# Kernel optimization log

Hardware: AMD Instinct MI355X
Metric: run time of the kernel (lower is better)

## Reference

```python
import jax, jax.numpy as jnp
import numpy as np

NUM_CLASSES = 22
SKIP = 20            # skip_pixels: stride over flattened pixel index
N_STEPS = 200        # discretized steps along each voting ray
STEP = 4.0           # pixels per ray step
INLIER_T = 0.9       # inlier_threshold on direction dot-product
LABEL_T = 500.0      # label_threshold: min #pixels of a class to be valid


def _hough_forward(label_2d, vertex_pred, extents, poses, meta_data):
    B, H, W = label_2d.shape
    C = NUM_CLASSES
    HW = H * W

    # ---- strided pixel sampling (skip_pixels) ----
    idx = jnp.arange(0, HW, SKIP)                      # [P]
    P = idx.shape[0]
    ys = (idx // W).astype(jnp.float32)                # [P]
    xs = (idx % W).astype(jnp.float32)
    labels = label_2d.reshape(B, HW)[:, idx].astype(jnp.int32)   # [B,P]
    vp = vertex_pred.reshape(B, HW, C, 3)[:, idx]                # [B,P,C,3]
    # pick each pixel's predicted (dx,dy,z) for its own class label
    sel = jnp.take_along_axis(
        vp, jnp.broadcast_to(labels[:, :, None, None], (B, P, 1, 3)), axis=2
    )[:, :, 0]                                                   # [B,P,3]
    d = sel[..., :2]
    dn = d / (jnp.linalg.norm(d, axis=-1, keepdims=True) + 1e-9)  # unit dir [B,P,2]
    z = sel[..., 2]                                               # [B,P]
    fg = labels > 0                                               # foreground mask

    # ---- ray voting into per-class Hough accumulator ----
    t = (jnp.arange(N_STEPS, dtype=jnp.float32) + 1.0) * STEP     # [T]
    cx = xs[None, :, None] + dn[..., 0:1] * t[None, None, :]      # [B,P,T]
    cy = ys[None, :, None] + dn[..., 1:2] * t[None, None, :]
    cxi = jnp.round(cx).astype(jnp.int32)
    cyi = jnp.round(cy).astype(jnp.int32)
    inb = (cxi >= 0) & (cxi < W) & (cyi >= 0) & (cyi < H) & fg[..., None]
    cxi = jnp.clip(cxi, 0, W - 1)
    cyi = jnp.clip(cyi, 0, H - 1)
    bidx = jnp.arange(B, dtype=jnp.int32)[:, None, None]
    flat = ((bidx * C + labels[:, :, None]) * H + cyi) * W + cxi  # [B,P,T]
    hough = jnp.zeros((B * C * HW,), jnp.float32)
    hough = hough.at[flat.reshape(-1)].add(inb.reshape(-1).astype(jnp.float32))
    hough = hough.reshape(B, C, H, W)

    # ---- per-class peak ----
    hflat = hough.reshape(B, C, HW)
    vmax = hflat.max(-1)                               # [B,C]
    pk = jnp.argmax(hflat, axis=-1).astype(jnp.int32)  # [B,C]
    pky = (pk // W).astype(jnp.float32)
    pkx = (pk % W).astype(jnp.float32)

    # ---- validity: enough labeled pixels for the class ----
    b2 = jnp.arange(B, dtype=jnp.int32)[:, None]
    counts = jnp.zeros((B, C), jnp.float32).at[
        jnp.broadcast_to(b2, (B, HW)).reshape(-1),
        label_2d.reshape(-1).astype(jnp.int32),
    ].add(1.0)                                          # [B,C] full-res pixel counts
    cls_ids = jnp.arange(C, dtype=jnp.float32)
    valid = (counts >= LABEL_T) & (cls_ids[None, :] > 0)  # [B,C]

    # ---- inlier selection + inlier-averaged depth ----
    cx_c = jnp.take_along_axis(pkx, labels, axis=1)    # [B,P] peak of pixel's class
    cy_c = jnp.take_along_axis(pky, labels, axis=1)
    dvec = jnp.stack([cx_c - xs[None, :], cy_c - ys[None, :]], axis=-1)
    dvec = dvec / (jnp.linalg.norm(dvec, axis=-1, keepdims=True) + 1e-9)
    dot = jnp.sum(dn * dvec, axis=-1)                  # [B,P]
    inl = (fg & (dot > INLIER_T)).astype(jnp.float32)  # [B,P]
    bP = jnp.broadcast_to(b2, (B, P)).reshape(-1)
    z_sum = jnp.zeros((B, C), jnp.float32).at[bP, labels.reshape(-1)].add((z * inl).reshape(-1))
    n_inl = jnp.zeros((B, C), jnp.float32).at[bP, labels.reshape(-1)].add(inl.reshape(-1))
    depth = z_sum / jnp.maximum(n_inl, 1.0)            # [B,C]
    z_safe = jnp.where(jnp.abs(depth) > 1e-3, depth, 1.0)

    # ---- bbox from extents + intrinsics ----
    fx = meta_data[:, 0:1]                             # [B,1]
    fy = meta_data[:, 4:5]
    diam = jnp.linalg.norm(extents, axis=-1)[None, :]  # [1,C]
    half_w = 0.5 * diam * fx / z_safe
    half_h = 0.5 * diam * fy / z_safe
    vmask = valid.astype(jnp.float32)
    rois = jnp.stack([
        jnp.broadcast_to(b2.astype(jnp.float32), (B, C)),
        jnp.broadcast_to(cls_ids[None, :], (B, C)),
        pkx - half_w, pky - half_h, pkx + half_w, pky + half_h,
        vmax,
    ], axis=-1) * vmask[..., None]                     # [B,C,7]

    # ---- pose init: identity quaternion + backprojected translation ----
    Kinv = meta_data[:, 9:18].reshape(B, 3, 3)
    hom = jnp.stack([pkx, pky, jnp.ones_like(pkx)], axis=-1)      # [B,C,3]
    ray = jnp.einsum('bij,bcj->bci', Kinv, hom)
    T = depth[..., None] * ray                                    # [B,C,3]
    quat = jnp.broadcast_to(jnp.array([1.0, 0.0, 0.0, 0.0], jnp.float32), (B, C, 4))
    pose_out = jnp.concatenate([quat, T], axis=-1) * vmask[..., None]  # [B,C,7]

    return jnp.concatenate([rois, pose_out], axis=-1)  # [B,C,14]


def setup_inputs() -> dict:
    key = jax.random.key(0)
    k1, k2, k3 = jax.random.split(key, 3)
    B, H, W = 2, 480, 640
    label_2d = jax.random.randint(k1, (B, H, W), 0, NUM_CLASSES, dtype=jnp.int32)
    vertex_pred = jax.random.normal(k2, (B, H, W, 3 * NUM_CLASSES), dtype=jnp.float32)
    extents = jax.random.uniform(k3, (NUM_CLASSES, 3), minval=0.05, maxval=0.3, dtype=jnp.float32)
    poses = jnp.zeros((B, 13), jnp.float32)
    K = np.array([[1066.778, 0, 312.9869], [0, 1067.487, 241.3109], [0, 0, 1]], dtype=np.float32)
    Kinv = np.linalg.pinv(K).astype(np.float32)
    md = np.zeros((B, 48), np.float32)
    md[:, 0:9] = K.flatten()
    md[:, 9:18] = Kinv.flatten()
    meta_data = jnp.asarray(md)
    return {"label_2d": label_2d, "vertex_pred": vertex_pred, "extents": extents,
            "poses": poses, "meta_data": meta_data}


def reference(label_2d, vertex_pred, extents, poses, meta_data):
    return _hough_forward(label_2d, vertex_pred, extents, poses, meta_data)
```

## Files before the change

### kernel.cpp

```cpp
#include <hip/hip_runtime.h>
#include <math.h>

#define C_      22
#define SKIP_   20
#define NSTEP_  200
#define STEP_   4.0f
#define INL_T_  0.9f
#define LAB_T_  500
#define B_      2
#define H_      480
#define W_      640
#define HW_     (H_ * W_)
#define P_      (HW_ / SKIP_)

#define TS_       64
#define TILES_X_  (W_ / TS_)
#define NTILES_Y_ 8
#define NTILES_   (TILES_X_ * NTILES_Y_)
#define NPLANES_  (B_ * (C_ - 1))
#define NPT_      (NPLANES_ * NTILES_)
#define CAP_      2048

#define SUB_A_    8
#define SEG_LEN_  (NSTEP_ / SUB_A_)
#define PA_BLOCKS_    ((B_ * P_ * SUB_A_) / 256)
#define HIST_BLOCKS_  ((B_ * HW_) / (256 * 4))
#define INL_BLOCKS_   ((B_ * P_) / 256)

#define KEY_INIT_ 0x00000000FFFFFFFFull

__device__ __forceinline__ void emit_run(unsigned int* cnt, uint4* lists, int pt,
                                         int xi, int yi, int i0, int i1,
                                         float dnx, float dny) {
    unsigned slot = atomicAdd(&cnt[pt], 1u);
    if (slot < CAP_) {
        uint4 r;
        r.x = (unsigned)xi | ((unsigned)yi << 16);
        r.y = (unsigned)i0 | ((unsigned)i1 << 8);
        r.z = __float_as_uint(dnx);
        r.w = __float_as_uint(dny);
        lists[(size_t)pt * CAP_ + slot] = r;
    }
}

__global__ __launch_bounds__(256) void binray_count_kernel(const int* __restrict__ label,
                                                           const float* __restrict__ vp,
                                                           unsigned int* __restrict__ cnt,
                                                           uint4* __restrict__ lists,
                                                           int* __restrict__ counts,
                                                           unsigned long long* __restrict__ key) {
    if (blockIdx.x < PA_BLOCKS_) {
        int tid = blockIdx.x * 256 + threadIdx.x;
        int pt  = tid >> 3;
        int sub = tid & 7;
        int b   = pt / P_;
        int pi  = pt - b * P_;
        int idx = pi * SKIP_;
        int lab = label[b * HW_ + idx];
        if (lab <= 0) return;
        int xi = idx % W_, yi = idx / W_;
        float xs = (float)xi, ys = (float)yi;
        const float* s = vp + ((size_t)(b * HW_ + idx) * (C_ * 3)) + lab * 3;
        float dx = s[0], dy = s[1];
        float nrm = sqrtf(__fadd_rn(__fmul_rn(dx, dx), __fmul_rn(dy, dy))) + 1e-9f;
        float dnx = dx / nrm, dny = dy / nrm;
        int base = (b * (C_ - 1) + (lab - 1)) * NTILES_;
        int curTile = -1, runStart = 0;
        bool entered = false;
        int iBeg = sub * SEG_LEN_, iEnd = iBeg + SEG_LEN_;
        for (int i = iBeg; i < iEnd; ++i) {
            float t = (float)(i + 1) * STEP_;
            float cx = __fadd_rn(xs, __fmul_rn(dnx, t));
            float cy = __fadd_rn(ys, __fmul_rn(dny, t));
            float cxr = rintf(cx);
            float cyr = rintf(cy);
            int tl2 = -1;
            if (cxr >= 0.0f && cxr <= (float)(W_ - 1) && cyr >= 0.0f && cyr <= (float)(H_ - 1))
                tl2 = (((int)cyr) >> 6) * TILES_X_ + (((int)cxr) >> 6);
            if (tl2 != curTile) {
                if (curTile >= 0)
                    emit_run(cnt, lists, base + curTile, xi, yi, runStart, i - 1, dnx, dny);
                curTile = tl2;
                runStart = i;
            }
            if (tl2 >= 0) entered = true;
            else if (entered) break;
        }
        if (curTile >= 0)
            emit_run(cnt, lists, base + curTile, xi, yi, runStart, iEnd - 1, dnx, dny);
    } else {
        __shared__ int h[C_];
        int cb  = blockIdx.x - PA_BLOCKS_;
        if (cb == 0 && threadIdx.x < B_ * C_)
            key[threadIdx.x] = KEY_INIT_;
        const int bpb = HW_ / 1024;
        int b   = cb / bpb;
        int off = (cb % bpb) * 1024 + threadIdx.x * 4;
        if (threadIdx.x < C_) h[threadIdx.x] = 0;
        __syncthreads();
        int4 l4 = *(const int4*)(label + b * HW_ + off);
        atomicAdd(&h[l4.x], 1);
        atomicAdd(&h[l4.y], 1);
        atomicAdd(&h[l4.z], 1);
        atomicAdd(&h[l4.w], 1);
        __syncthreads();
        if (threadIdx.x < C_) {
            int v = h[threadIdx.x];
            if (v) atomicAdd(&counts[b * C_ + threadIdx.x], v);
        }
    }
}

__global__ __launch_bounds__(256) void raster_argmax_kernel(const unsigned int* __restrict__ cnt,
                                                            const uint4* __restrict__ lists,
                                                            unsigned long long* __restrict__ key) {
    __shared__ unsigned int tile[TS_ * TS_ / 2];
    __shared__ unsigned int sv[256];
    __shared__ int          si[256];
    int pt = blockIdx.x;
    int n = (int)cnt[pt];
    if (n == 0) return;
    if (n > CAP_) n = CAP_;
    {
        uint4* t4 = (uint4*)tile;
        t4[threadIdx.x]       = make_uint4(0u, 0u, 0u, 0u);
        t4[threadIdx.x + 256] = make_uint4(0u, 0u, 0u, 0u);
    }
    __syncthreads();
    int p  = pt / NTILES_;
    int tl = pt % NTILES_;
    int b = p / (C_ - 1);
    int c = p % (C_ - 1) + 1;
    int x0 = (tl % TILES_X_) * TS_;
    int y0 = (tl / TILES_X_) * TS_;
    const uint4* lst = lists + (size_t)pt * CAP_;
    int hwv = threadIdx.x >> 5, ln = threadIdx.x & 31;
    for (int r = hwv; r < n; r += 8) {
        uint4 rec = lst[r];
        int i0 = (int)(rec.y & 0xFFu), i1 = (int)((rec.y >> 8) & 0xFFu);
        float xs = (float)(rec.x & 0xFFFFu);
        float ys = (float)(rec.x >> 16);
        float dnx = __uint_as_float(rec.z);
        float dny = __uint_as_float(rec.w);
        for (int i = i0 + ln; i <= i1; i += 32) {
            float t = (float)(i + 1) * STEP_;
            float cx = __fadd_rn(xs, __fmul_rn(dnx, t));
            float cy = __fadd_rn(ys, __fmul_rn(dny, t));
            int lx = (int)rintf(cx) - x0;
            int ly = (int)rintf(cy) - y0;
            int cell = ly * TS_ + lx;
            atomicAdd(&tile[cell >> 1], 1u << ((cell & 1) * 16));
        }
    }
    __syncthreads();
    unsigned bv = 0u; int bi = 0;
    {
        unsigned w0 = tile[threadIdx.x];
        bv = w0 & 0xFFFFu; bi = threadIdx.x * 2;
        unsigned hi = w0 >> 16;
        if (hi > bv) { bv = hi; bi = threadIdx.x * 2 + 1; }
    }
    #pragma unroll
    for (int j = 1; j < 8; ++j) {
        int ix = threadIdx.x + j * 256;
        unsigned w = tile[ix];
        unsigned lo = w & 0xFFFFu, hi = w >> 16;
        if (lo > bv) { bv = lo; bi = ix * 2; }
        if (hi > bv) { bv = hi; bi = ix * 2 + 1; }
    }
    sv[threadIdx.x] = bv; si[threadIdx.x] = bi;
    __syncthreads();
    for (int s = 128; s > 0; s >>= 1) {
        if (threadIdx.x < s) {
            unsigned ov = sv[threadIdx.x + s]; int oi = si[threadIdx.x + s];
            if (ov > sv[threadIdx.x] || (ov == sv[threadIdx.x] && oi < si[threadIdx.x])) {
                sv[threadIdx.x] = ov; si[threadIdx.x] = oi;
            }
        }
        __syncthreads();
    }
    if (threadIdx.x == 0) {
        int ly = si[0] >> 6, lx = si[0] & 63;
        unsigned gidx = (unsigned)((y0 + ly) * W_ + (x0 + lx));
        unsigned long long k = ((unsigned long long)sv[0] << 32)
                             | (unsigned long long)(0xFFFFFFFFu - gidx);
        atomicMax(&key[b * C_ + c], k);
    }
}

__global__ __launch_bounds__(256) void inlier_finalize_kernel(const int* __restrict__ label,
                                                              const float* __restrict__ vp,
                                                              const unsigned long long* __restrict__ key,
                                                              float* __restrict__ z_sum,
                                                              float* __restrict__ n_inl,
                                                              int* __restrict__ counts,
                                                              const float* __restrict__ extents,
                                                              const float* __restrict__ meta,
                                                              unsigned int* __restrict__ done,
                                                              float* __restrict__ out) {
    __shared__ float zs[C_];
    __shared__ float ns[C_];
    __shared__ int last_flag;
    const int bpb = P_ / 256;
    int b  = blockIdx.x / bpb;
    int pi = (blockIdx.x % bpb) * 256 + threadIdx.x;
    if (threadIdx.x < C_) { zs[threadIdx.x] = 0.0f; ns[threadIdx.x] = 0.0f; }
    __syncthreads();
    int idx = pi * SKIP_;
    int lab = label[b * HW_ + idx];
    if (lab > 0) {
        float ys = (float)(idx / W_);
        float xs = (float)(idx % W_);
        const float* s = vp + ((size_t)(b * HW_ + idx) * (C_ * 3)) + lab * 3;
        float dx = s[0], dy = s[1], z = s[2];
        float nrm = sqrtf(__fadd_rn(__fmul_rn(dx, dx), __fmul_rn(dy, dy))) + 1e-9f;
        float dnx = dx / nrm, dny = dy / nrm;
        unsigned long long k = key[b * C_ + lab];
        int pkv = (int)(0xFFFFFFFFu - (unsigned int)(k & 0xFFFFFFFFull));
        float pkx = (float)(pkv % W_), pky = (float)(pkv / W_);
        float dvx = __fsub_rn(pkx, xs), dvy = __fsub_rn(pky, ys);
        float nrm2 = sqrtf(__fadd_rn(__fmul_rn(dvx, dvx), __fmul_rn(dvy, dvy))) + 1e-9f;
        dvx /= nrm2; dvy /= nrm2;
        float dot = __fadd_rn(__fmul_rn(dnx, dvx), __fmul_rn(dny, dvy));
        if (dot > INL_T_) {
            atomicAdd(&zs[lab], z);
            atomicAdd(&ns[lab], 1.0f);
        }
    }
    __syncthreads();
    if (threadIdx.x < C_) {
        if (ns[threadIdx.x] != 0.0f) {
            atomicAdd(&z_sum[b * C_ + threadIdx.x], zs[threadIdx.x]);
            atomicAdd(&n_inl[b * C_ + threadIdx.x], ns[threadIdx.x]);
        }
    }
    if (threadIdx.x == 0) {
        __threadfence();
        unsigned prev = atomicAdd(done, 1u);
        last_flag = (prev == (unsigned)(INL_BLOCKS_ - 1)) ? 1 : 0;
    }
    __syncthreads();
    if (!last_flag) return;
    __threadfence();
    int t = threadIdx.x;
    if (t >= B_ * C_) return;
    int bb = t / C_, c = t % C_;
    float* o = out + t * 14;
    int   cnt_t  = atomicAdd(&counts[t], 0);
    float zsum_t = atomicAdd(&z_sum[t], 0.0f);
    float ninl_t = atomicAdd(&n_inl[t], 0.0f);
    unsigned long long k = atomicAdd((unsigned long long*)&key[0] + t, 0ull);
    bool valid = (cnt_t >= LAB_T_) && (c > 0);
    if (!valid) {
        #pragma unroll
        for (int k2 = 0; k2 < 14; ++k2) o[k2] = 0.0f;
        return;
    }
    float depth = zsum_t / fmaxf(ninl_t, 1.0f);
    float z_safe = (fabsf(depth) > 0.001f) ? depth : 1.0f;
    float fx = meta[bb * 48 + 0];
    float fy = meta[bb * 48 + 4];
    const float* e = extents + c * 3;
    float diam = sqrtf(e[0]*e[0] + e[1]*e[1] + e[2]*e[2]);
    float vmax = (float)(unsigned int)(k >> 32);
    int pkv = (int)(0xFFFFFFFFu - (unsigned int)(k & 0xFFFFFFFFull));
    float pkx = (float)(pkv % W_), pky = (float)(pkv / W_);
    float half_w = ((0.5f * diam) * fx) / z_safe;
    float half_h = ((0.5f * diam) * fy) / z_safe;
    o[0] = (float)bb;
    o[1] = (float)c;
    o[2] = pkx - half_w;
    o[3] = pky - half_h;
    o[4] = pkx + half_w;
    o[5] = pky + half_h;
    o[6] = vmax;
    const float* Ki = meta + bb * 48 + 9;
    float rx = Ki[0]*pkx + Ki[1]*pky + Ki[2];
    float ry = Ki[3]*pkx + Ki[4]*pky + Ki[5];
    float rz = Ki[6]*pkx + Ki[7]*pky + Ki[8];
    o[7]  = 1.0f;
    o[8]  = 0.0f;
    o[9]  = 0.0f;
    o[10] = 0.0f;
    o[11] = depth * rx;
    o[12] = depth * ry;
    o[13] = depth * rz;
}

extern "C" void kernel_launch(void* const* d_in, const int* in_sizes, int n_in,
                              void* d_out, int out_size, void* d_ws, size_t ws_size,
                              hipStream_t stream) {
    const int*   label   = (const int*)d_in[0];
    const float* vp      = (const float*)d_in[1];
    const float* extents = (const float*)d_in[2];
    const float* meta    = (const float*)d_in[4];
    float* out = (float*)d_out;

    char* ws = (char*)d_ws;
    size_t off = 0;
    unsigned int* cnt = (unsigned int*)(ws + off);  off += NPT_ * sizeof(unsigned int);
    int*   counts = (int*)(ws + off);   off += B_ * C_ * sizeof(int);
    float* z_sum  = (float*)(ws + off); off += B_ * C_ * sizeof(float);
    float* n_inl  = (float*)(ws + off); off += B_ * C_ * sizeof(float);
    unsigned int* done = (unsigned int*)(ws + off); off += sizeof(unsigned int);
    size_t zero_bytes = off;
    off = (off + 15) & ~(size_t)15;
    unsigned long long* key = (unsigned long long*)(ws + off);
    off += B_ * C_ * sizeof(unsigned long long);
    off = (off + 15) & ~(size_t)15;
    uint4* lists = (uint4*)(ws + off);

    hipMemsetAsync(d_ws, 0, zero_bytes, stream);

    binray_count_kernel<<<PA_BLOCKS_ + HIST_BLOCKS_, 256, 0, stream>>>(label, vp, cnt, lists, counts, key);
    raster_argmax_kernel<<<NPT_, 256, 0, stream>>>(cnt, lists, key);
    inlier_finalize_kernel<<<INL_BLOCKS_, 256, 0, stream>>>(label, vp, key, z_sum, n_inl,
                                                            counts, extents, meta, done, out);
}
```

Before: 259.4 us.

## Replace memset and three launches with two kernels using in-kernel flag synchronization

Drops the workspace memset by having block 0 of the first kernel zero the counters and publish magic flags. The other blocks spin on those flags before doing their work. The first kernel becomes persistent with a fixed 1024-block grid, and the raster/argmax and inlier/finalize kernels merge into one launch whose inlier blocks spin until every raster tile has signalled completion. The aim is to save launch and memset overhead, but it relies on forward progress of spinning blocks and adds busy-wait costs.

```diff
diff --git a/kernel.cpp b/kernel.cpp
--- a/kernel.cpp
+++ b/kernel.cpp
@@ -25,9 +25,13 @@
 #define SEG_LEN_  (NSTEP_ / SUB_A_)
 #define PA_BLOCKS_    ((B_ * P_ * SUB_A_) / 256)
 #define HIST_BLOCKS_  ((B_ * HW_) / (256 * 4))
+#define UNITS1_       (PA_BLOCKS_ + HIST_BLOCKS_)
+#define GRID1_        1024
 #define INL_BLOCKS_   ((B_ * P_) / 256)
 
 #define KEY_INIT_ 0x00000000FFFFFFFFull
+#define MAGIC1_   0x9E3779B9u
+#define MAGIC2_   0x61C8C646u
 
 __device__ __forceinline__ void emit_run(unsigned int* cnt, uint4* lists, int pt,
                                          int xi, int yi, int i0, int i1,
@@ -43,168 +47,217 @@
     }
 }
 
-__global__ __launch_bounds__(256) void binray_count_kernel(const int* __restrict__ label,
-                                                           const float* __restrict__ vp,
-                                                           unsigned int* __restrict__ cnt,
-                                                           uint4* __restrict__ lists,
-                                                           int* __restrict__ counts,
-                                                           unsigned long long* __restrict__ key) {
-    if (blockIdx.x < PA_BLOCKS_) {
-        int tid = blockIdx.x * 256 + threadIdx.x;
-        int pt  = tid >> 3;
-        int sub = tid & 7;
-        int b   = pt / P_;
-        int pi  = pt - b * P_;
-        int idx = pi * SKIP_;
-        int lab = label[b * HW_ + idx];
-        if (lab <= 0) return;
-        int xi = idx % W_, yi = idx / W_;
-        float xs = (float)xi, ys = (float)yi;
-        const float* s = vp + ((size_t)(b * HW_ + idx) * (C_ * 3)) + lab * 3;
-        float dx = s[0], dy = s[1];
-        float nrm = sqrtf(__fadd_rn(__fmul_rn(dx, dx), __fmul_rn(dy, dy))) + 1e-9f;
-        float dnx = dx / nrm, dny = dy / nrm;
-        int base = (b * (C_ - 1) + (lab - 1)) * NTILES_;
-        int curTile = -1, runStart = 0;
-        bool entered = false;
-        int iBeg = sub * SEG_LEN_, iEnd = iBeg + SEG_LEN_;
-        for (int i = iBeg; i < iEnd; ++i) {
-            float t = (float)(i + 1) * STEP_;
-            float cx = __fadd_rn(xs, __fmul_rn(dnx, t));
-            float cy = __fadd_rn(ys, __fmul_rn(dny, t));
-            float cxr = rintf(cx);
-            float cyr = rintf(cy);
-            int tl2 = -1;
-            if (cxr >= 0.0f && cxr <= (float)(W_ - 1) && cyr >= 0.0f && cyr <= (float)(H_ - 1))
-                tl2 = (((int)cyr) >> 6) * TILES_X_ + (((int)cxr) >> 6);
-            if (tl2 != curTile) {
+__global__ __launch_bounds__(256, 4) void binray_init_kernel(const int* __restrict__ label,
+                                                             const float* __restrict__ vp,
+                                                             unsigned int* __restrict__ cnt,
+                                                             uint4* __restrict__ lists,
+                                                             int* __restrict__ counts,
+                                                             float* __restrict__ z_sum,
+                                                             float* __restrict__ n_inl,
+                                                             unsigned int* __restrict__ done,
+                                                             unsigned int* __restrict__ rdone,
+                                                             unsigned int* __restrict__ flags,
+                                                             unsigned long long* __restrict__ key) {
+    __shared__ int h[C_];
+    const int tid = threadIdx.x;
+    if (blockIdx.x == 0) {
+        for (int i = tid; i < NPT_; i += 256) cnt[i] = 0u;
+        if (tid < B_ * C_) {
+            counts[tid] = 0;
+            z_sum[tid] = 0.0f;
+            n_inl[tid] = 0.0f;
+            key[tid] = KEY_INIT_;
+        }
+        if (tid == 0) { *done = 0u; *rdone = 0u; }
+        __syncthreads();
+        __threadfence();
+        if (tid == 0) {
+            atomicExch(&flags[0], MAGIC1_);
+            atomicExch(&flags[1], MAGIC2_);
+        }
+        __syncthreads();
+    } else {
+        if (tid == 0) {
+            while (true) {
+                unsigned f1 = atomicAdd(&flags[0], 0u);
+                unsigned f2 = atomicAdd(&flags[1], 0u);
+                if (f1 == MAGIC1_ && f2 == MAGIC2_) break;
+                __builtin_amdgcn_s_sleep(2);
+            }
+            __threadfence();
+        }
+        __syncthreads();
+    }
+
+    for (int u = blockIdx.x; u < UNITS1_; u += GRID1_) {
+        if (u < PA_BLOCKS_) {
+            int t0  = u * 256 + tid;
+            int pt  = t0 >> 3;
+            int sub = t0 & 7;
+            int b   = pt / P_;
+            int pi  = pt - b * P_;
+            int idx = pi * SKIP_;
+            int lab = label[b * HW_ + idx];
+            if (lab > 0) {
+                int xi = idx % W_, yi = idx / W_;
+                float xs = (float)xi, ys = (float)yi;
+                const float* s = vp + ((size_t)(b * HW_ + idx) * (C_ * 3)) + lab * 3;
+                float dx = s[0], dy = s[1];
+                float nrm = sqrtf(__fadd_rn(__fmul_rn(dx, dx), __fmul_rn(dy, dy))) + 1e-9f;
+                float dnx = dx / nrm, dny = dy / nrm;
+                int base = (b * (C_ - 1) + (lab - 1)) * NTILES_;
+                int curTile = -1, runStart = 0;
+                bool entered = false;
+                int iBeg = sub * SEG_LEN_, iEnd = iBeg + SEG_LEN_;
+                for (int i = iBeg; i < iEnd; ++i) {
+                    float t = (float)(i + 1) * STEP_;
+                    float cx = __fadd_rn(xs, __fmul_rn(dnx, t));
+                    float cy = __fadd_rn(ys, __fmul_rn(dny, t));
+                    float cxr = rintf(cx);
+                    float cyr = rintf(cy);
+                    int tl2 = -1;
+                    if (cxr >= 0.0f && cxr <= (float)(W_ - 1) && cyr >= 0.0f && cyr <= (float)(H_ - 1))
+                        tl2 = (((int)cyr) >> 6) * TILES_X_ + (((int)cxr) >> 6);
+                    if (tl2 != curTile) {
+                        if (curTile >= 0)
+                            emit_run(cnt, lists, base + curTile, xi, yi, runStart, i - 1, dnx, dny);
+                        curTile = tl2;
+                        runStart = i;
+                    }
+                    if (tl2 >= 0) entered = true;
+                    else if (entered) break;
+                }
                 if (curTile >= 0)
-                    emit_run(cnt, lists, base + curTile, xi, yi, runStart, i - 1, dnx, dny);
-                curTile = tl2;
-                runStart = i;
-            }
-            if (tl2 >= 0) entered = true;
-            else if (entered) break;
-        }
-        if (curTile >= 0)
-            emit_run(cnt, lists, base + curTile, xi, yi, runStart, iEnd - 1, dnx, dny);
-    } else {
-        __shared__ int h[C_];
-        int cb  = blockIdx.x - PA_BLOCKS_;
-        if (cb == 0 && threadIdx.x < B_ * C_)
-            key[threadIdx.x] = KEY_INIT_;
-        const int bpb = HW_ / 1024;
-        int b   = cb / bpb;
-        int off = (cb % bpb) * 1024 + threadIdx.x * 4;
-        if (threadIdx.x < C_) h[threadIdx.x] = 0;
-        __syncthreads();
-        int4 l4 = *(const int4*)(label + b * HW_ + off);
-        atomicAdd(&h[l4.x], 1);
-        atomicAdd(&h[l4.y], 1);
-        atomicAdd(&h[l4.z], 1);
-        atomicAdd(&h[l4.w], 1);
-        __syncthreads();
-        if (threadIdx.x < C_) {
-            int v = h[threadIdx.x];
-            if (v) atomicAdd(&counts[b * C_ + threadIdx.x], v);
+                    emit_run(cnt, lists, base + curTile, xi, yi, runStart, iEnd - 1, dnx, dny);
+            }
+        } else {
+            int cb  = u - PA_BLOCKS_;
+            const int bpb = HW_ / 1024;
+            int b   = cb / bpb;
+            int off = (cb % bpb) * 1024 + tid * 4;
+            if (tid < C_) h[tid] = 0;
+            __syncthreads();
+            int4 l4 = *(const int4*)(label + b * HW_ + off);
+            atomicAdd(&h[l4.x], 1);
+            atomicAdd(&h[l4.y], 1);
+            atomicAdd(&h[l4.z], 1);
+            atomicAdd(&h[l4.w], 1);
+            __syncthreads();
+            if (tid < C_) {
+                int v = h[tid];
+                if (v) atomicAdd(&counts[b * C_ + tid], v);
+            }
+            __syncthreads();
         }
     }
 }
 
-__global__ __launch_bounds__(256) void raster_argmax_kernel(const unsigned int* __restrict__ cnt,
-                                                            const uint4* __restrict__ lists,
-                                                            unsigned long long* __restrict__ key) {
-    __shared__ unsigned int tile[TS_ * TS_ / 2];
-    __shared__ unsigned int sv[256];
-    __shared__ int          si[256];
-    int pt = blockIdx.x;
-    int n = (int)cnt[pt];
-    if (n == 0) return;
-    if (n > CAP_) n = CAP_;
-    {
-        uint4* t4 = (uint4*)tile;
-        t4[threadIdx.x]       = make_uint4(0u, 0u, 0u, 0u);
-        t4[threadIdx.x + 256] = make_uint4(0u, 0u, 0u, 0u);
+__global__ __launch_bounds__(256) void raster_inlier_finalize_kernel(
+        const unsigned int* __restrict__ cnt, const uint4* __restrict__ lists,
+        unsigned long long* __restrict__ key,
+        const int* __restrict__ label, const float* __restrict__ vp,
+        float* __restrict__ z_sum, float* __restrict__ n_inl,
+        int* __restrict__ counts, const float* __restrict__ extents,
+        const float* __restrict__ meta,
+        unsigned int* __restrict__ done, unsigned int* __restrict__ rdone,
+        unsigned int* __restrict__ flags, float* __restrict__ out) {
+    __shared__ union {
+        struct { unsigned int tile[TS_ * TS_ / 2]; unsigned int sv[256]; int si[256]; } rb;
+        struct { float zs[C_]; float ns[C_]; unsigned long long kk[C_]; int last_flag; } in;
+    } sm;
+    const int tid = threadIdx.x;
+
+    if (blockIdx.x < NPT_) {
+        int pt = blockIdx.x;
+        int n = (int)cnt[pt];
+        if (n == 0) {
+            if (tid == 0) atomicAdd(rdone, 1u);
+            return;
+        }
+        if (n > CAP_) n = CAP_;
+        {
+            uint4* t4 = (uint4*)sm.rb.tile;
+            t4[tid]       = make_uint4(0u, 0u, 0u, 0u);
+            t4[tid + 256] = make_uint4(0u, 0u, 0u, 0u);
+        }
+        __syncthreads();
+        int p  = pt / NTILES_;
+        int tl = pt % NTILES_;
+        int b = p / (C_ - 1);
+        int c = p % (C_ - 1) + 1;
+        int x0 = (tl % TILES_X_) * TS_;
+        int y0 = (tl / TILES_X_) * TS_;
+        const uint4* lst = lists + (size_t)pt * CAP_;
+        int hwv = tid >> 5, ln = tid & 31;
+        for (int r = hwv; r < n; r += 8) {
+            uint4 rec = lst[r];
+            int i0 = (int)(rec.y & 0xFFu), i1 = (int)((rec.y >> 8) & 0xFFu);
+            float xs = (float)(rec.x & 0xFFFFu);
+            float ys = (float)(rec.x >> 16);
+            float dnx = __uint_as_float(rec.z);
+            float dny = __uint_as_float(rec.w);
+            for (int i = i0 + ln; i <= i1; i += 32) {
+                float t = (float)(i + 1) * STEP_;
+                float cx = __fadd_rn(xs, __fmul_rn(dnx, t));
+                float cy = __fadd_rn(ys, __fmul_rn(dny, t));
+                int lx = (int)rintf(cx) - x0;
+                int ly = (int)rintf(cy) - y0;
+                int cell = ly * TS_ + lx;
+                atomicAdd(&sm.rb.tile[cell >> 1], 1u << ((cell & 1) * 16));
+            }
+        }
+        __syncthreads();
+        unsigned bv = 0u; int bi = 0;
+        {
+            unsigned w0 = sm.rb.tile[tid];
+            bv = w0 & 0xFFFFu; bi = tid * 2;
+            unsigned hi = w0 >> 16;
+            if (hi > bv) { bv = hi; bi = tid * 2 + 1; }
+        }
+        #pragma unroll
+        for (int j = 1; j < 8; ++j) {
+            int ix = tid + j * 256;
+            unsigned w = sm.rb.tile[ix];
+            unsigned lo = w & 0xFFFFu, hi = w >> 16;
+            if (lo > bv) { bv = lo; bi = ix * 2; }
+            if (hi > bv) { bv = hi; bi = ix * 2 + 1; }
+        }
+        sm.rb.sv[tid] = bv; sm.rb.si[tid] = bi;
+        __syncthreads();
+        for (int s = 128; s > 0; s >>= 1) {
+            if (tid < s) {
+                unsigned ov = sm.rb.sv[tid + s]; int oi = sm.rb.si[tid + s];
+                if (ov > sm.rb.sv[tid] || (ov == sm.rb.sv[tid] && oi < sm.rb.si[tid])) {
+                    sm.rb.sv[tid] = ov; sm.rb.si[tid] = oi;
+                }
+            }
+            __syncthreads();
+        }
+        if (tid == 0) {
+            int ly = sm.rb.si[0] >> 6, lx = sm.rb.si[0] & 63;
+            unsigned gidx = (unsigned)((y0 + ly) * W_ + (x0 + lx));
+            unsigned long long k = ((unsigned long long)sm.rb.sv[0] << 32)
+                                 | (unsigned long long)(0xFFFFFFFFu - gidx);
+            atomicMax(&key[b * C_ + c], k);
+            __threadfence();
+            atomicAdd(rdone, 1u);
+        }
+        return;
+    }
+
+    int ib = blockIdx.x - NPT_;
+    const int bpb = P_ / 256;
+    int b  = ib / bpb;
+    int pi = (ib % bpb) * 256 + tid;
+    if (tid == 0) {
+        while (atomicAdd(rdone, 0u) < (unsigned)NPT_) __builtin_amdgcn_s_sleep(8);
+        __threadfence();
     }
     __syncthreads();
-    int p  = pt / NTILES_;
-    int tl = pt % NTILES_;
-    int b = p / (C_ - 1);
-    int c = p % (C_ - 1) + 1;
-    int x0 = (tl % TILES_X_) * TS_;
-    int y0 = (tl / TILES_X_) * TS_;
-    const uint4* lst = lists + (size_t)pt * CAP_;
-    int hwv = threadIdx.x >> 5, ln = threadIdx.x & 31;
-    for (int r = hwv; r < n; r += 8) {
-        uint4 rec = lst[r];
-        int i0 = (int)(rec.y & 0xFFu), i1 = (int)((rec.y >> 8) & 0xFFu);
-        float xs = (float)(rec.x & 0xFFFFu);
-        float ys = (float)(rec.x >> 16);
-        float dnx = __uint_as_float(rec.z);
-        float dny = __uint_as_float(rec.w);
-        for (int i = i0 + ln; i <= i1; i += 32) {
-            float t = (float)(i + 1) * STEP_;
-            float cx = __fadd_rn(xs, __fmul_rn(dnx, t));
-            float cy = __fadd_rn(ys, __fmul_rn(dny, t));
-            int lx = (int)rintf(cx) - x0;
-            int ly = (int)rintf(cy) - y0;
-            int cell = ly * TS_ + lx;
-            atomicAdd(&tile[cell >> 1], 1u << ((cell & 1) * 16));
-        }
-    }
-    __syncthreads();
-    unsigned bv = 0u; int bi = 0;
-    {
-        unsigned w0 = tile[threadIdx.x];
-        bv = w0 & 0xFFFFu; bi = threadIdx.x * 2;
-        unsigned hi = w0 >> 16;
-        if (hi > bv) { bv = hi; bi = threadIdx.x * 2 + 1; }
-    }
-    #pragma unroll
-    for (int j = 1; j < 8; ++j) {
-        int ix = threadIdx.x + j * 256;
-        unsigned w = tile[ix];
-        unsigned lo = w & 0xFFFFu, hi = w >> 16;
-        if (lo > bv) { bv = lo; bi = ix * 2; }
-        if (hi > bv) { bv = hi; bi = ix * 2 + 1; }
-    }
-    sv[threadIdx.x] = bv; si[threadIdx.x] = bi;
-    __syncthreads();
-    for (int s = 128; s > 0; s >>= 1) {
-        if (threadIdx.x < s) {
-            unsigned ov = sv[threadIdx.x + s]; int oi = si[threadIdx.x + s];
-            if (ov > sv[threadIdx.x] || (ov == sv[threadIdx.x] && oi < si[threadIdx.x])) {
-                sv[threadIdx.x] = ov; si[threadIdx.x] = oi;
-            }
-        }
-        __syncthreads();
-    }
-    if (threadIdx.x == 0) {
-        int ly = si[0] >> 6, lx = si[0] & 63;
-        unsigned gidx = (unsigned)((y0 + ly) * W_ + (x0 + lx));
-        unsigned long long k = ((unsigned long long)sv[0] << 32)
-                             | (unsigned long long)(0xFFFFFFFFu - gidx);
-        atomicMax(&key[b * C_ + c], k);
-    }
-}
-
-__global__ __launch_bounds__(256) void inlier_finalize_kernel(const int* __restrict__ label,
-                                                              const float* __restrict__ vp,
-                                                              const unsigned long long* __restrict__ key,
-                                                              float* __restrict__ z_sum,
-                                                              float* __restrict__ n_inl,
-                                                              int* __restrict__ counts,
-                                                              const float* __restrict__ extents,
-                                                              const float* __restrict__ meta,
-                                                              unsigned int* __restrict__ done,
-                                                              float* __restrict__ out) {
-    __shared__ float zs[C_];
-    __shared__ float ns[C_];
-    __shared__ int last_flag;
-    const int bpb = P_ / 256;
-    int b  = blockIdx.x / bpb;
-    int pi = (blockIdx.x % bpb) * 256 + threadIdx.x;
-    if (threadIdx.x < C_) { zs[threadIdx.x] = 0.0f; ns[threadIdx.x] = 0.0f; }
+    if (tid < C_) {
+        sm.in.zs[tid] = 0.0f; sm.in.ns[tid] = 0.0f;
+        sm.in.kk[tid] = atomicAdd(&key[b * C_ + tid], 0ull);
+    }
     __syncthreads();
     int idx = pi * SKIP_;
     int lab = label[b * HW_ + idx];
@@ -215,7 +268,7 @@
         float dx = s[0], dy = s[1], z = s[2];
         float nrm = sqrtf(__fadd_rn(__fmul_rn(dx, dx), __fmul_rn(dy, dy))) + 1e-9f;
         float dnx = dx / nrm, dny = dy / nrm;
-        unsigned long long k = key[b * C_ + lab];
+        unsigned long long k = sm.in.kk[lab];
         int pkv = (int)(0xFFFFFFFFu - (unsigned int)(k & 0xFFFFFFFFull));
         float pkx = (float)(pkv % W_), pky = (float)(pkv / W_);
         float dvx = __fsub_rn(pkx, xs), dvy = __fsub_rn(pky, ys);
@@ -223,33 +276,37 @@
         dvx /= nrm2; dvy /= nrm2;
         float dot = __fadd_rn(__fmul_rn(dnx, dvx), __fmul_rn(dny, dvy));
         if (dot > INL_T_) {
-            atomicAdd(&zs[lab], z);
-            atomicAdd(&ns[lab], 1.0f);
+            atomicAdd(&sm.in.zs[lab], z);
+            atomicAdd(&sm.in.ns[lab], 1.0f);
         }
     }
     __syncthreads();
-    if (threadIdx.x < C_) {
-        if (ns[threadIdx.x] != 0.0f) {
-            atomicAdd(&z_sum[b * C_ + threadIdx.x], zs[threadIdx.x]);
-            atomicAdd(&n_inl[b * C_ + threadIdx.x], ns[threadIdx.x]);
-        }
-    }
-    if (threadIdx.x == 0) {
+    if (tid < C_) {
+        if (sm.in.ns[tid] != 0.0f) {
+            atomicAdd(&z_sum[b * C_ + tid], sm.in.zs[tid]);
+            atomicAdd(&n_inl[b * C_ + tid], sm.in.ns[tid]);
+        }
+    }
+    if (tid == 0) {
         __threadfence();
         unsigned prev = atomicAdd(done, 1u);
-        last_flag = (prev == (unsigned)(INL_BLOCKS_ - 1)) ? 1 : 0;
+        sm.in.last_flag = (prev == (unsigned)(INL_BLOCKS_ - 1)) ? 1 : 0;
     }
     __syncthreads();
-    if (!last_flag) return;
+    if (!sm.in.last_flag) return;
     __threadfence();
-    int t = threadIdx.x;
+    if (tid == 0) {
+        atomicExch(&flags[0], 0u);
+        atomicExch(&flags[1], 0u);
+    }
+    int t = tid;
     if (t >= B_ * C_) return;
     int bb = t / C_, c = t % C_;
     float* o = out + t * 14;
     int   cnt_t  = atomicAdd(&counts[t], 0);
     float zsum_t = atomicAdd(&z_sum[t], 0.0f);
     float ninl_t = atomicAdd(&n_inl[t], 0.0f);
-    unsigned long long k = atomicAdd((unsigned long long*)&key[0] + t, 0ull);
+    unsigned long long k = atomicAdd(&key[t], 0ull);
     bool valid = (cnt_t >= LAB_T_) && (c > 0);
     if (!valid) {
         #pragma unroll
@@ -302,18 +359,18 @@
     int*   counts = (int*)(ws + off);   off += B_ * C_ * sizeof(int);
     float* z_sum  = (float*)(ws + off); off += B_ * C_ * sizeof(float);
     float* n_inl  = (float*)(ws + off); off += B_ * C_ * sizeof(float);
-    unsigned int* done = (unsigned int*)(ws + off); off += sizeof(unsigned int);
-    size_t zero_bytes = off;
+    unsigned int* done  = (unsigned int*)(ws + off); off += sizeof(unsigned int);
+    unsigned int* rdone = (unsigned int*)(ws + off); off += sizeof(unsigned int);
+    unsigned int* flags = (unsigned int*)(ws + off); off += 2 * sizeof(unsigned int);
     off = (off + 15) & ~(size_t)15;
     unsigned long long* key = (unsigned long long*)(ws + off);
     off += B_ * C_ * sizeof(unsigned long long);
     off = (off + 15) & ~(size_t)15;
     uint4* lists = (uint4*)(ws + off);
 
-    hipMemsetAsync(d_ws, 0, zero_bytes, stream);
-
-    binray_count_kernel<<<PA_BLOCKS_ + HIST_BLOCKS_, 256, 0, stream>>>(label, vp, cnt, lists, counts, key);
-    raster_argmax_kernel<<<NPT_, 256, 0, stream>>>(cnt, lists, key);
-    inlier_finalize_kernel<<<INL_BLOCKS_, 256, 0, stream>>>(label, vp, key, z_sum, n_inl,
-                                                            counts, extents, meta, done, out);
+    binray_init_kernel<<<GRID1_, 256, 0, stream>>>(label, vp, cnt, lists, counts,
+                                                   z_sum, n_inl, done, rdone, flags, key);
+    raster_inlier_finalize_kernel<<<NPT_ + INL_BLOCKS_, 256, 0, stream>>>(
+        cnt, lists, key, label, vp, z_sum, n_inl, counts, extents, meta,
+        done, rdone, flags, out);
 }
```

Result: slower. 398.3 us (+53.5%).

## Fuse inlier voting into raster kernel via per-class pixel lists and last-block finalize

Applied to the files above, without the earlier changes.

The first kernel now also writes each foreground pixel's position, depth and unit direction into a per-class compacted list. The inlier/finalize kernel is removed. The last raster block to finish for each class plane, detected with a per-plane done counter, reads that list to accumulate inlier depth and write the output row. The argmax reduction uses wave shuffles instead of a shared-memory tree. This removes one kernel launch and avoids re-reading labels and the strided vertex predictions, at the cost of extra global writes in the first kernel, and the per-class inlier pass now runs serially inside a single block.

```diff
diff --git a/kernel.cpp b/kernel.cpp
--- a/kernel.cpp
+++ b/kernel.cpp
@@ -25,7 +25,6 @@
 #define SEG_LEN_  (NSTEP_ / SUB_A_)
 #define PA_BLOCKS_    ((B_ * P_ * SUB_A_) / 256)
 #define HIST_BLOCKS_  ((B_ * HW_) / (256 * 4))
-#define INL_BLOCKS_   ((B_ * P_) / 256)
 
 #define KEY_INIT_ 0x00000000FFFFFFFFull
 
@@ -48,7 +47,10 @@
                                                            unsigned int* __restrict__ cnt,
                                                            uint4* __restrict__ lists,
                                                            int* __restrict__ counts,
-                                                           unsigned long long* __restrict__ key) {
+                                                           unsigned int* __restrict__ cls_cnt,
+                                                           uint4* __restrict__ cls,
+                                                           unsigned long long* __restrict__ key,
+                                                           float* __restrict__ out) {
     if (blockIdx.x < PA_BLOCKS_) {
         int tid = blockIdx.x * 256 + threadIdx.x;
         int pt  = tid >> 3;
@@ -64,7 +66,20 @@
         float dx = s[0], dy = s[1];
         float nrm = sqrtf(__fadd_rn(__fmul_rn(dx, dx), __fmul_rn(dy, dy))) + 1e-9f;
         float dnx = dx / nrm, dny = dy / nrm;
-        int base = (b * (C_ - 1) + (lab - 1)) * NTILES_;
+        int p = b * (C_ - 1) + (lab - 1);
+        int base = p * NTILES_;
+        if (sub == 0) {
+            float z = s[2];
+            unsigned slot = atomicAdd(&cls_cnt[p], 1u);
+            if (slot < (unsigned)P_) {
+                uint4 r;
+                r.x = (unsigned)xi | ((unsigned)yi << 16);
+                r.y = __float_as_uint(z);
+                r.z = __float_as_uint(dnx);
+                r.w = __float_as_uint(dny);
+                cls[(size_t)p * P_ + slot] = r;
+            }
+        }
         int curTile = -1, runStart = 0;
         bool entered = false;
         int iBeg = sub * SEG_LEN_, iEnd = iBeg + SEG_LEN_;
@@ -91,8 +106,14 @@
     } else {
         __shared__ int h[C_];
         int cb  = blockIdx.x - PA_BLOCKS_;
-        if (cb == 0 && threadIdx.x < B_ * C_)
-            key[threadIdx.x] = KEY_INIT_;
+        if (cb == 0) {
+            if (threadIdx.x < B_ * C_)
+                key[threadIdx.x] = KEY_INIT_;
+            else if (threadIdx.x < B_ * C_ + 14)
+                out[threadIdx.x - B_ * C_] = 0.0f;
+            else if (threadIdx.x < B_ * C_ + 28)
+                out[C_ * 14 + (threadIdx.x - B_ * C_ - 14)] = 0.0f;
+        }
         const int bpb = HW_ / 1024;
         int b   = cb / bpb;
         int off = (cb % bpb) * 1024 + threadIdx.x * 4;
@@ -111,146 +132,140 @@
     }
 }
 
-__global__ __launch_bounds__(256) void raster_argmax_kernel(const unsigned int* __restrict__ cnt,
-                                                            const uint4* __restrict__ lists,
-                                                            unsigned long long* __restrict__ key) {
-    __shared__ unsigned int tile[TS_ * TS_ / 2];
-    __shared__ unsigned int sv[256];
-    __shared__ int          si[256];
+__global__ __launch_bounds__(256) void raster_finalize_kernel(
+        const unsigned int* __restrict__ cnt, const uint4* __restrict__ lists,
+        unsigned long long* __restrict__ key,
+        const uint4* __restrict__ cls, const unsigned int* __restrict__ cls_cnt,
+        unsigned int* __restrict__ pdone,
+        const int* __restrict__ counts, const float* __restrict__ extents,
+        const float* __restrict__ meta, float* __restrict__ out) {
+    __shared__ union {
+        struct { unsigned int tile[TS_ * TS_ / 2]; unsigned int sv[4]; int si[4]; } rb;
+        struct { float zp[4]; float np[4]; } in;
+    } sm;
+    __shared__ int last_flag;
+    __shared__ unsigned long long kbro;
+    const int tid = threadIdx.x;
+
     int pt = blockIdx.x;
-    int n = (int)cnt[pt];
-    if (n == 0) return;
-    if (n > CAP_) n = CAP_;
-    {
-        uint4* t4 = (uint4*)tile;
-        t4[threadIdx.x]       = make_uint4(0u, 0u, 0u, 0u);
-        t4[threadIdx.x + 256] = make_uint4(0u, 0u, 0u, 0u);
-    }
-    __syncthreads();
     int p  = pt / NTILES_;
     int tl = pt % NTILES_;
     int b = p / (C_ - 1);
     int c = p % (C_ - 1) + 1;
     int x0 = (tl % TILES_X_) * TS_;
     int y0 = (tl / TILES_X_) * TS_;
-    const uint4* lst = lists + (size_t)pt * CAP_;
-    int hwv = threadIdx.x >> 5, ln = threadIdx.x & 31;
-    for (int r = hwv; r < n; r += 8) {
-        uint4 rec = lst[r];
-        int i0 = (int)(rec.y & 0xFFu), i1 = (int)((rec.y >> 8) & 0xFFu);
+
+    int n = (int)cnt[pt];
+    if (n > CAP_) n = CAP_;
+    if (n > 0) {
+        {
+            uint4* t4 = (uint4*)sm.rb.tile;
+            t4[tid]       = make_uint4(0u, 0u, 0u, 0u);
+            t4[tid + 256] = make_uint4(0u, 0u, 0u, 0u);
+        }
+        __syncthreads();
+        const uint4* lst = lists + (size_t)pt * CAP_;
+        int hwv = tid >> 5, ln = tid & 31;
+        for (int r = hwv; r < n; r += 8) {
+            uint4 rec = lst[r];
+            int i0 = (int)(rec.y & 0xFFu), i1 = (int)((rec.y >> 8) & 0xFFu);
+            float xs = (float)(rec.x & 0xFFFFu);
+            float ys = (float)(rec.x >> 16);
+            float dnx = __uint_as_float(rec.z);
+            float dny = __uint_as_float(rec.w);
+            for (int i = i0 + ln; i <= i1; i += 32) {
+                float t = (float)(i + 1) * STEP_;
+                float cx = __fadd_rn(xs, __fmul_rn(dnx, t));
+                float cy = __fadd_rn(ys, __fmul_rn(dny, t));
+                int lx = (int)rintf(cx) - x0;
+                int ly = (int)rintf(cy) - y0;
+                int cell = ly * TS_ + lx;
+                atomicAdd(&sm.rb.tile[cell >> 1], 1u << ((cell & 1) * 16));
+            }
+        }
+        __syncthreads();
+        unsigned bv = 0u; int bi = 0;
+        {
+            unsigned w0 = sm.rb.tile[tid];
+            bv = w0 & 0xFFFFu; bi = tid * 2;
+            unsigned hi = w0 >> 16;
+            if (hi > bv) { bv = hi; bi = tid * 2 + 1; }
+        }
+        #pragma unroll
+        for (int j = 1; j < 8; ++j) {
+            int ix = tid + j * 256;
+            unsigned w = sm.rb.tile[ix];
+            unsigned lo = w & 0xFFFFu, hi = w >> 16;
+            if (lo > bv) { bv = lo; bi = ix * 2; }
+            if (hi > bv) { bv = hi; bi = ix * 2 + 1; }
+        }
+        #pragma unroll
+        for (int s = 1; s < 64; s <<= 1) {
+            unsigned ov = (unsigned)__shfl_xor((int)bv, s);
+            int      oi = __shfl_xor(bi, s);
+            if (ov > bv || (ov == bv && oi < bi)) { bv = ov; bi = oi; }
+        }
+        if ((tid & 63) == 0) { sm.rb.sv[tid >> 6] = bv; sm.rb.si[tid >> 6] = bi; }
+        __syncthreads();
+        if (tid == 0) {
+            unsigned fbv = sm.rb.sv[0]; int fbi = sm.rb.si[0];
+            #pragma unroll
+            for (int w = 1; w < 4; ++w) {
+                unsigned ov = sm.rb.sv[w]; int oi = sm.rb.si[w];
+                if (ov > fbv || (ov == fbv && oi < fbi)) { fbv = ov; fbi = oi; }
+            }
+            int ly = fbi >> 6, lx = fbi & 63;
+            unsigned gidx = (unsigned)((y0 + ly) * W_ + (x0 + lx));
+            unsigned long long k = ((unsigned long long)fbv << 32)
+                                 | (unsigned long long)(0xFFFFFFFFu - gidx);
+            atomicMax(&key[b * C_ + c], k);
+        }
+    }
+
+    if (tid == 0) {
+        __threadfence();
+        unsigned prev = atomicAdd(&pdone[p], 1u);
+        last_flag = (prev == (unsigned)(NTILES_ - 1)) ? 1 : 0;
+    }
+    __syncthreads();
+    if (!last_flag) return;
+    __threadfence();
+    if (tid == 0) kbro = atomicAdd(&key[b * C_ + c], 0ull);
+    __syncthreads();
+    unsigned long long k = kbro;
+    int pkv = (int)(0xFFFFFFFFu - (unsigned int)(k & 0xFFFFFFFFull));
+    float pkx = (float)(pkv % W_), pky = (float)(pkv / W_);
+
+    int m = (int)cls_cnt[p];
+    if (m > P_) m = P_;
+    const uint4* cl = cls + (size_t)p * P_;
+    float zacc = 0.0f, nacc = 0.0f;
+    for (int r = tid; r < m; r += 256) {
+        uint4 rec = cl[r];
         float xs = (float)(rec.x & 0xFFFFu);
         float ys = (float)(rec.x >> 16);
+        float z   = __uint_as_float(rec.y);
         float dnx = __uint_as_float(rec.z);
         float dny = __uint_as_float(rec.w);
-        for (int i = i0 + ln; i <= i1; i += 32) {
-            float t = (float)(i + 1) * STEP_;
-            float cx = __fadd_rn(xs, __fmul_rn(dnx, t));
-            float cy = __fadd_rn(ys, __fmul_rn(dny, t));
-            int lx = (int)rintf(cx) - x0;
-            int ly = (int)rintf(cy) - y0;
-            int cell = ly * TS_ + lx;
-            atomicAdd(&tile[cell >> 1], 1u << ((cell & 1) * 16));
-        }
-    }
-    __syncthreads();
-    unsigned bv = 0u; int bi = 0;
-    {
-        unsigned w0 = tile[threadIdx.x];
-        bv = w0 & 0xFFFFu; bi = threadIdx.x * 2;
-        unsigned hi = w0 >> 16;
-        if (hi > bv) { bv = hi; bi = threadIdx.x * 2 + 1; }
-    }
-    #pragma unroll
-    for (int j = 1; j < 8; ++j) {
-        int ix = threadIdx.x + j * 256;
-        unsigned w = tile[ix];
-        unsigned lo = w & 0xFFFFu, hi = w >> 16;
-        if (lo > bv) { bv = lo; bi = ix * 2; }
-        if (hi > bv) { bv = hi; bi = ix * 2 + 1; }
-    }
-    sv[threadIdx.x] = bv; si[threadIdx.x] = bi;
-    __syncthreads();
-    for (int s = 128; s > 0; s >>= 1) {
-        if (threadIdx.x < s) {
-            unsigned ov = sv[threadIdx.x + s]; int oi = si[threadIdx.x + s];
-            if (ov > sv[threadIdx.x] || (ov == sv[threadIdx.x] && oi < si[threadIdx.x])) {
-                sv[threadIdx.x] = ov; si[threadIdx.x] = oi;
-            }
-        }
-        __syncthreads();
-    }
-    if (threadIdx.x == 0) {
-        int ly = si[0] >> 6, lx = si[0] & 63;
-        unsigned gidx = (unsigned)((y0 + ly) * W_ + (x0 + lx));
-        unsigned long long k = ((unsigned long long)sv[0] << 32)
-                             | (unsigned long long)(0xFFFFFFFFu - gidx);
-        atomicMax(&key[b * C_ + c], k);
-    }
-}
-
-__global__ __launch_bounds__(256) void inlier_finalize_kernel(const int* __restrict__ label,
-                                                              const float* __restrict__ vp,
-                                                              const unsigned long long* __restrict__ key,
-                                                              float* __restrict__ z_sum,
-                                                              float* __restrict__ n_inl,
-                                                              int* __restrict__ counts,
-                                                              const float* __restrict__ extents,
-                                                              const float* __restrict__ meta,
-                                                              unsigned int* __restrict__ done,
-                                                              float* __restrict__ out) {
-    __shared__ float zs[C_];
-    __shared__ float ns[C_];
-    __shared__ int last_flag;
-    const int bpb = P_ / 256;
-    int b  = blockIdx.x / bpb;
-    int pi = (blockIdx.x % bpb) * 256 + threadIdx.x;
-    if (threadIdx.x < C_) { zs[threadIdx.x] = 0.0f; ns[threadIdx.x] = 0.0f; }
-    __syncthreads();
-    int idx = pi * SKIP_;
-    int lab = label[b * HW_ + idx];
-    if (lab > 0) {
-        float ys = (float)(idx / W_);
-        float xs = (float)(idx % W_);
-        const float* s = vp + ((size_t)(b * HW_ + idx) * (C_ * 3)) + lab * 3;
-        float dx = s[0], dy = s[1], z = s[2];
-        float nrm = sqrtf(__fadd_rn(__fmul_rn(dx, dx), __fmul_rn(dy, dy))) + 1e-9f;
-        float dnx = dx / nrm, dny = dy / nrm;
-        unsigned long long k = key[b * C_ + lab];
-        int pkv = (int)(0xFFFFFFFFu - (unsigned int)(k & 0xFFFFFFFFull));
-        float pkx = (float)(pkv % W_), pky = (float)(pkv / W_);
         float dvx = __fsub_rn(pkx, xs), dvy = __fsub_rn(pky, ys);
         float nrm2 = sqrtf(__fadd_rn(__fmul_rn(dvx, dvx), __fmul_rn(dvy, dvy))) + 1e-9f;
         dvx /= nrm2; dvy /= nrm2;
         float dot = __fadd_rn(__fmul_rn(dnx, dvx), __fmul_rn(dny, dvy));
-        if (dot > INL_T_) {
-            atomicAdd(&zs[lab], z);
-            atomicAdd(&ns[lab], 1.0f);
-        }
-    }
+        if (dot > INL_T_) { zacc += z; nacc += 1.0f; }
+    }
+    #pragma unroll
+    for (int s = 1; s < 64; s <<= 1) {
+        zacc += __shfl_xor(zacc, s);
+        nacc += __shfl_xor(nacc, s);
+    }
+    if ((tid & 63) == 0) { sm.in.zp[tid >> 6] = zacc; sm.in.np[tid >> 6] = nacc; }
     __syncthreads();
-    if (threadIdx.x < C_) {
-        if (ns[threadIdx.x] != 0.0f) {
-            atomicAdd(&z_sum[b * C_ + threadIdx.x], zs[threadIdx.x]);
-            atomicAdd(&n_inl[b * C_ + threadIdx.x], ns[threadIdx.x]);
-        }
-    }
-    if (threadIdx.x == 0) {
-        __threadfence();
-        unsigned prev = atomicAdd(done, 1u);
-        last_flag = (prev == (unsigned)(INL_BLOCKS_ - 1)) ? 1 : 0;
-    }
-    __syncthreads();
-    if (!last_flag) return;
-    __threadfence();
-    int t = threadIdx.x;
-    if (t >= B_ * C_) return;
-    int bb = t / C_, c = t % C_;
-    float* o = out + t * 14;
-    int   cnt_t  = atomicAdd(&counts[t], 0);
-    float zsum_t = atomicAdd(&z_sum[t], 0.0f);
-    float ninl_t = atomicAdd(&n_inl[t], 0.0f);
-    unsigned long long k = atomicAdd((unsigned long long*)&key[0] + t, 0ull);
-    bool valid = (cnt_t >= LAB_T_) && (c > 0);
+    if (tid != 0) return;
+
+    float zsum_t = sm.in.zp[0] + sm.in.zp[1] + sm.in.zp[2] + sm.in.zp[3];
+    float ninl_t = sm.in.np[0] + sm.in.np[1] + sm.in.np[2] + sm.in.np[3];
+    float* o = out + (b * C_ + c) * 14;
+    bool valid = (counts[b * C_ + c] >= LAB_T_);
     if (!valid) {
         #pragma unroll
         for (int k2 = 0; k2 < 14; ++k2) o[k2] = 0.0f;
@@ -258,23 +273,21 @@
     }
     float depth = zsum_t / fmaxf(ninl_t, 1.0f);
     float z_safe = (fabsf(depth) > 0.001f) ? depth : 1.0f;
-    float fx = meta[bb * 48 + 0];
-    float fy = meta[bb * 48 + 4];
+    float fx = meta[b * 48 + 0];
+    float fy = meta[b * 48 + 4];
     const float* e = extents + c * 3;
     float diam = sqrtf(e[0]*e[0] + e[1]*e[1] + e[2]*e[2]);
     float vmax = (float)(unsigned int)(k >> 32);
-    int pkv = (int)(0xFFFFFFFFu - (unsigned int)(k & 0xFFFFFFFFull));
-    float pkx = (float)(pkv % W_), pky = (float)(pkv / W_);
     float half_w = ((0.5f * diam) * fx) / z_safe;
     float half_h = ((0.5f * diam) * fy) / z_safe;
-    o[0] = (float)bb;
+    o[0] = (float)b;
     o[1] = (float)c;
     o[2] = pkx - half_w;
     o[3] = pky - half_h;
     o[4] = pkx + half_w;
     o[5] = pky + half_h;
     o[6] = vmax;
-    const float* Ki = meta + bb * 48 + 9;
+    const float* Ki = meta + b * 48 + 9;
     float rx = Ki[0]*pkx + Ki[1]*pky + Ki[2];
     float ry = Ki[3]*pkx + Ki[4]*pky + Ki[5];
     float rz = Ki[6]*pkx + Ki[7]*pky + Ki[8];
@@ -298,22 +311,24 @@
 
     char* ws = (char*)d_ws;
     size_t off = 0;
-    unsigned int* cnt = (unsigned int*)(ws + off);  off += NPT_ * sizeof(unsigned int);
-    int*   counts = (int*)(ws + off);   off += B_ * C_ * sizeof(int);
-    float* z_sum  = (float*)(ws + off); off += B_ * C_ * sizeof(float);
-    float* n_inl  = (float*)(ws + off); off += B_ * C_ * sizeof(float);
-    unsigned int* done = (unsigned int*)(ws + off); off += sizeof(unsigned int);
+    unsigned int* cnt     = (unsigned int*)(ws + off); off += NPT_ * sizeof(unsigned int);
+    int*          counts  = (int*)(ws + off);          off += B_ * C_ * sizeof(int);
+    unsigned int* cls_cnt = (unsigned int*)(ws + off); off += NPLANES_ * sizeof(unsigned int);
+    unsigned int* pdone   = (unsigned int*)(ws + off); off += NPLANES_ * sizeof(unsigned int);
     size_t zero_bytes = off;
     off = (off + 15) & ~(size_t)15;
     unsigned long long* key = (unsigned long long*)(ws + off);
     off += B_ * C_ * sizeof(unsigned long long);
     off = (off + 15) & ~(size_t)15;
     uint4* lists = (uint4*)(ws + off);
+    off += (size_t)NPT_ * CAP_ * sizeof(uint4);
+    uint4* cls = (uint4*)(ws + off);
+    off += (size_t)NPLANES_ * P_ * sizeof(uint4);
 
     hipMemsetAsync(d_ws, 0, zero_bytes, stream);
 
-    binray_count_kernel<<<PA_BLOCKS_ + HIST_BLOCKS_, 256, 0, stream>>>(label, vp, cnt, lists, counts, key);
-    raster_argmax_kernel<<<NPT_, 256, 0, stream>>>(cnt, lists, key);
-    inlier_finalize_kernel<<<INL_BLOCKS_, 256, 0, stream>>>(label, vp, key, z_sum, n_inl,
-                                                            counts, extents, meta, done, out);
+    binray_count_kernel<<<PA_BLOCKS_ + HIST_BLOCKS_, 256, 0, stream>>>(
+        label, vp, cnt, lists, counts, cls_cnt, cls, key, out);
+    raster_finalize_kernel<<<NPT_, 256, 0, stream>>>(
+        cnt, lists, key, cls, cls_cnt, pdone, counts, extents, meta, out);
 }
```

New measurement: 380.5 us. +46.7%, slower.
